# Performance work log

Measured on AMD Instinct MI355X. Metric: run time of the kernel, lower is better.

The kernel has to match this reference:

```python
import jax, jax.numpy as jnp
import numpy as np

G = 8   # channel groups
K = 4   # top-k per group


def setup_inputs() -> dict:
    key = jax.random.key(0)
    ks = jax.random.split(key, 6)
    B, C, H, W = 16, 256, 128, 128
    x = jax.random.normal(ks[0], (B, C, H, W), dtype=jnp.float32)
    # 1x1 conv weights (kernel dims squeezed):
    soft_w1 = jax.random.normal(ks[1], (G, C // G), dtype=jnp.float32) * 0.1  # grouped Conv2d(C, G, 1, groups=G)
    soft_w2 = jax.random.normal(ks[2], (C, G), dtype=jnp.float32) * 0.1       # Conv2d(G, C, 1)
    top_w1 = jax.random.normal(ks[3], (G, K), dtype=jnp.float32) * 0.1        # grouped Conv2d(G*K, G, 1, groups=G)
    top_w2 = jax.random.normal(ks[4], (C, G), dtype=jnp.float32) * 0.1        # Conv2d(G, C, 1)
    r = jax.random.normal(ks[5], (2,), dtype=jnp.float32)                     # branch mixing logits
    return {"x": x, "soft_w1": soft_w1, "soft_w2": soft_w2,
            "top_w1": top_w1, "top_w2": top_w2, "r": r}


def reference(x, soft_w1, soft_w2, top_w1, top_w2, r):
    B, C, H, W = x.shape
    Cg = C // G
    xg = x.reshape(B, G, Cg, H, W)

    # --- CGSoftmax branch: x + conv2(conv1(x * softmax_per_group(x))) ---
    att = jax.nn.softmax(xg, axis=2)          # softmax over within-group channels
    xs = xg * att                              # MulRes
    y = jnp.einsum('bgchw,gc->bghw', xs, soft_w1)     # grouped 1x1 conv C->G
    soft_out = x + jnp.einsum('bghw,og->bohw', y, soft_w2)  # 1x1 conv G->C, AddRes

    # --- CGTopK branch: x + conv2(conv1(topk_per_group(x))) ---
    tk = -jnp.sort(-xg, axis=2)[:, :, :K]      # top-K values, sorted descending: [B,G,K,H,W]
    yt = jnp.einsum('bgkhw,gk->bghw', tk, top_w1)     # grouped 1x1 conv G*K->G
    top_out = x + jnp.einsum('bghw,og->bohw', yt, top_w2)  # 1x1 conv G->C, AddRes

    # --- softmax-weighted branch combine ---
    w = jax.nn.softmax(r)
    rt, rs = w[0], w[1]
    return top_out * rt + soft_out * rs
```

## Files before the change

### kernel.cpp

```cpp
#include <hip/hip_runtime.h>
#include <math.h>


#define G_ 8
#define K_ 4
#define CG_ 32
#define C_ 256
#define HW_ (128 * 128)

typedef __attribute__((ext_vector_type(2))) float f32x2;

__launch_bounds__(512, 4)
__global__ void cgblock_kernel(const float* __restrict__ x,
                               const float* __restrict__ soft_w1,
                               const float* __restrict__ soft_w2,
                               const float* __restrict__ top_w1,
                               const float* __restrict__ top_w2,
                               const float* __restrict__ r,
                               float* __restrict__ out) {
    __shared__ f32x2 Ys[G_][64];
    __shared__ f32x2 Yt[G_][64];

    const int lane = threadIdx.x & 63;
    const int g = __builtin_amdgcn_readfirstlane(threadIdx.x >> 6);
    const int blk = blockIdx.x;
    const int b = blk >> 7;
    const int s = ((blk & 127) << 7) | (lane << 1);

    const long base = (long)(b * C_ + g * CG_) * HW_ + s;
    const f32x2* xp = (const f32x2*)(x + base);

    const float e0 = __expf(r[0]);
    const float e1 = __expf(r[1]);
    const float rt = e0 / (e0 + e1);
    const float rs = e1 / (e0 + e1);

    float va[CG_], vb[CG_];
#pragma unroll
    for (int c = 0; c < CG_; ++c) {
        const f32x2 L = __builtin_nontemporal_load(xp + c * (HW_ / 2));
        va[c] = L.x;
        vb[c] = L.y;
    }

    float ma = va[0], mb = vb[0];
#pragma unroll
    for (int c = 1; c < CG_; ++c) {
        ma = fmaxf(ma, va[c]);
        mb = fmaxf(mb, vb[c]);
    }
    float Za = 0.f, Zb = 0.f, aa = 0.f, ab = 0.f;
#pragma unroll
    for (int c = 0; c < CG_; ++c) {
        const float w1 = soft_w1[g * CG_ + c];
        const float ea = __expf(va[c] - ma);
        const float eb = __expf(vb[c] - mb);
        Za += ea;
        Zb += eb;
        aa = fmaf(va[c] * ea, w1, aa);
        ab = fmaf(vb[c] * eb, w1, ab);
    }
    const float ysa = aa / Za;
    const float ysb = ab / Zb;

    float a0 = -INFINITY, a1 = -INFINITY, a2 = -INFINITY, a3 = -INFINITY;
    float b0 = -INFINITY, b1 = -INFINITY, b2 = -INFINITY, b3 = -INFINITY;
#pragma unroll
    for (int c = 0; c < CG_; ++c) {
        float u = va[c];
        float d0 = fminf(a0, u); a0 = fmaxf(a0, u);
        float d1 = fminf(a1, d0); a1 = fmaxf(a1, d0);
        float d2 = fminf(a2, d1); a2 = fmaxf(a2, d1);
        a3 = fmaxf(a3, d2);
        u = vb[c];
        d0 = fminf(b0, u); b0 = fmaxf(b0, u);
        d1 = fminf(b1, d0); b1 = fmaxf(b1, d0);
        d2 = fminf(b2, d1); b2 = fmaxf(b2, d1);
        b3 = fmaxf(b3, d2);
    }
    const float tw0 = top_w1[g * K_ + 0], tw1 = top_w1[g * K_ + 1];
    const float tw2 = top_w1[g * K_ + 2], tw3 = top_w1[g * K_ + 3];
    const float yta = a0 * tw0 + a1 * tw1 + a2 * tw2 + a3 * tw3;
    const float ytb = b0 * tw0 + b1 * tw1 + b2 * tw2 + b3 * tw3;

    Ys[g][lane] = f32x2{ysa * rs, ysb * rs};
    Yt[g][lane] = f32x2{yta * rt, ytb * rt};
    __syncthreads();

    const float* w2s = soft_w2 + g * CG_ * G_;
    const float* w2t = top_w2 + g * CG_ * G_;
#pragma unroll
    for (int gg = 0; gg < G_; ++gg) {
        const f32x2 yf = Ys[gg][lane];
        const f32x2 tf = Yt[gg][lane];
#pragma unroll
        for (int c = 0; c < CG_; ++c) {
            const float cs = w2s[c * G_ + gg];
            const float ct = w2t[c * G_ + gg];
            va[c] = fmaf(cs, yf.x, va[c]);
            vb[c] = fmaf(cs, yf.y, vb[c]);
            va[c] = fmaf(ct, tf.x, va[c]);
            vb[c] = fmaf(ct, tf.y, vb[c]);
        }
    }

    f32x2* op = (f32x2*)(out + base);
#pragma unroll
    for (int c = 0; c < CG_; ++c) {
        __builtin_nontemporal_store(f32x2{va[c], vb[c]}, op + c * (HW_ / 2));
    }
}

extern "C" void kernel_launch(void* const* d_in, const int* in_sizes, int n_in,
                              void* d_out, int out_size, void* d_ws, size_t ws_size,
                              hipStream_t stream) {
    const float* x       = (const float*)d_in[0];
    const float* soft_w1 = (const float*)d_in[1];
    const float* soft_w2 = (const float*)d_in[2];
    const float* top_w1  = (const float*)d_in[3];
    const float* top_w2  = (const float*)d_in[4];
    const float* r       = (const float*)d_in[5];
    float* out = (float*)d_out;

    cgblock_kernel<<<dim3(2048), dim3(512), 0, stream>>>(
        x, soft_w1, soft_w2, top_w1, top_w2, r, out);
}
```

Measured before the change: 443.4 us.

## Vectorize compute with packed f32x2 math, med3 top-k, and interleaved store loop

Rewrites the per-pixel math on f32x2 vectors so the compiler can emit packed FMA/max instructions, replaces the min/max top-4 insertion network with fmed3-based updates, and turns the max reduction into a tree. The Ys/Yt shared arrays are merged into a single f32x4 array that is read once into registers. The output loop is reordered to finish and store each channel in turn, which frees registers earlier and overlaps stores with compute. The kernel is memory-bound, so the gain from reduced ALU work may be small; the extra yv registers could raise register pressure.

Result: no change. 435.9 us (-1.7%).

```diff
diff --git a/kernel.cpp b/kernel.cpp
--- a/kernel.cpp
+++ b/kernel.cpp
@@ -9,6 +9,22 @@
 #define HW_ (128 * 128)
 
 typedef __attribute__((ext_vector_type(2))) float f32x2;
+typedef __attribute__((ext_vector_type(4))) float f32x4;
+
+static __device__ __forceinline__ f32x2 pk2(float s) { return f32x2{s, s}; }
+
+static __device__ __forceinline__ f32x2 maxv(f32x2 a, f32x2 b) {
+    return __builtin_elementwise_max(a, b);
+}
+
+static __device__ __forceinline__ f32x2 fmav(f32x2 a, f32x2 b, f32x2 c) {
+    return __builtin_elementwise_fma(a, b, c);
+}
+
+static __device__ __forceinline__ f32x2 med3v(f32x2 u, f32x2 x, f32x2 y) {
+    return f32x2{__builtin_amdgcn_fmed3f(u.x, x.x, y.x),
+                 __builtin_amdgcn_fmed3f(u.y, x.y, y.y)};
+}
 
 __launch_bounds__(512, 4)
 __global__ void cgblock_kernel(const float* __restrict__ x,
@@ -18,8 +34,7 @@
                                const float* __restrict__ top_w2,
                                const float* __restrict__ r,
                                float* __restrict__ out) {
-    __shared__ f32x2 Ys[G_][64];
-    __shared__ f32x2 Yt[G_][64];
+    __shared__ f32x4 Y[G_][64];
 
     const int lane = threadIdx.x & 63;
     const int g = __builtin_amdgcn_readfirstlane(threadIdx.x >> 6);
@@ -35,79 +50,76 @@
     const float rt = e0 / (e0 + e1);
     const float rs = e1 / (e0 + e1);
 
-    float va[CG_], vb[CG_];
+    f32x2 v[CG_];
 #pragma unroll
     for (int c = 0; c < CG_; ++c) {
-        const f32x2 L = __builtin_nontemporal_load(xp + c * (HW_ / 2));
-        va[c] = L.x;
-        vb[c] = L.y;
+        v[c] = __builtin_nontemporal_load(xp + c * (HW_ / 2));
     }
 
-    float ma = va[0], mb = vb[0];
+    f32x2 mm[16];
 #pragma unroll
-    for (int c = 1; c < CG_; ++c) {
-        ma = fmaxf(ma, va[c]);
-        mb = fmaxf(mb, vb[c]);
+    for (int i = 0; i < 16; ++i) mm[i] = maxv(v[i], v[i + 16]);
+#pragma unroll
+    for (int st = 8; st >= 1; st >>= 1) {
+#pragma unroll
+        for (int i = 0; i < st; ++i) mm[i] = maxv(mm[i], mm[i + st]);
     }
-    float Za = 0.f, Zb = 0.f, aa = 0.f, ab = 0.f;
+    const f32x2 m = mm[0];
+
+    f32x2 Z = pk2(0.f), acc = pk2(0.f);
 #pragma unroll
     for (int c = 0; c < CG_; ++c) {
         const float w1 = soft_w1[g * CG_ + c];
-        const float ea = __expf(va[c] - ma);
-        const float eb = __expf(vb[c] - mb);
-        Za += ea;
-        Zb += eb;
-        aa = fmaf(va[c] * ea, w1, aa);
-        ab = fmaf(vb[c] * eb, w1, ab);
+        const f32x2 d = v[c] - m;
+        const f32x2 e = f32x2{__expf(d.x), __expf(d.y)};
+        Z += e;
+        acc = fmav(v[c] * e, pk2(w1), acc);
     }
-    const float ysa = aa / Za;
-    const float ysb = ab / Zb;
+    const f32x2 ys = f32x2{acc.x / Z.x, acc.y / Z.y};
 
-    float a0 = -INFINITY, a1 = -INFINITY, a2 = -INFINITY, a3 = -INFINITY;
-    float b0 = -INFINITY, b1 = -INFINITY, b2 = -INFINITY, b3 = -INFINITY;
+    f32x2 A0 = pk2(-INFINITY), A1 = pk2(-INFINITY);
+    f32x2 A2 = pk2(-INFINITY), A3 = pk2(-INFINITY);
 #pragma unroll
     for (int c = 0; c < CG_; ++c) {
-        float u = va[c];
-        float d0 = fminf(a0, u); a0 = fmaxf(a0, u);
-        float d1 = fminf(a1, d0); a1 = fmaxf(a1, d0);
-        float d2 = fminf(a2, d1); a2 = fmaxf(a2, d1);
-        a3 = fmaxf(a3, d2);
-        u = vb[c];
-        d0 = fminf(b0, u); b0 = fmaxf(b0, u);
-        d1 = fminf(b1, d0); b1 = fmaxf(b1, d0);
-        d2 = fminf(b2, d1); b2 = fmaxf(b2, d1);
-        b3 = fmaxf(b3, d2);
+        const f32x2 u = v[c];
+        const f32x2 n0 = maxv(A0, u);
+        const f32x2 n1 = med3v(u, A0, A1);
+        const f32x2 n2 = med3v(u, A1, A2);
+        const f32x2 n3 = med3v(u, A2, A3);
+        A0 = n0; A1 = n1; A2 = n2; A3 = n3;
     }
     const float tw0 = top_w1[g * K_ + 0], tw1 = top_w1[g * K_ + 1];
     const float tw2 = top_w1[g * K_ + 2], tw3 = top_w1[g * K_ + 3];
-    const float yta = a0 * tw0 + a1 * tw1 + a2 * tw2 + a3 * tw3;
-    const float ytb = b0 * tw0 + b1 * tw1 + b2 * tw2 + b3 * tw3;
+    f32x2 yt = A3 * pk2(tw3);
+    yt = fmav(A2, pk2(tw2), yt);
+    yt = fmav(A1, pk2(tw1), yt);
+    yt = fmav(A0, pk2(tw0), yt);
 
-    Ys[g][lane] = f32x2{ysa * rs, ysb * rs};
-    Yt[g][lane] = f32x2{yta * rt, ytb * rt};
+    const f32x2 yss = ys * pk2(rs);
+    const f32x2 ytt = yt * pk2(rt);
+    Y[g][lane] = f32x4{yss.x, yss.y, ytt.x, ytt.y};
     __syncthreads();
 
+    f32x4 yv[G_];
+#pragma unroll
+    for (int gg = 0; gg < G_; ++gg) yv[gg] = Y[gg][lane];
+
+    f32x2* op = (f32x2*)(out + base);
     const float* w2s = soft_w2 + g * CG_ * G_;
     const float* w2t = top_w2 + g * CG_ * G_;
 #pragma unroll
-    for (int gg = 0; gg < G_; ++gg) {
-        const f32x2 yf = Ys[gg][lane];
-        const f32x2 tf = Yt[gg][lane];
+    for (int c = 0; c < CG_; ++c) {
+        f32x2 o = v[c];
 #pragma unroll
-        for (int c = 0; c < CG_; ++c) {
+        for (int gg = 0; gg < G_; ++gg) {
             const float cs = w2s[c * G_ + gg];
             const float ct = w2t[c * G_ + gg];
-            va[c] = fmaf(cs, yf.x, va[c]);
-            vb[c] = fmaf(cs, yf.y, vb[c]);
-            va[c] = fmaf(ct, tf.x, va[c]);
-            vb[c] = fmaf(ct, tf.y, vb[c]);
+            const f32x2 yf = f32x2{yv[gg].x, yv[gg].y};
+            const f32x2 tf = f32x2{yv[gg].z, yv[gg].w};
+            o = fmav(pk2(cs), yf, o);
+            o = fmav(pk2(ct), tf, o);
         }
-    }
-
-    f32x2* op = (f32x2*)(out + base);
-#pragma unroll
-    for (int c = 0; c < CG_; ++c) {
-        __builtin_nontemporal_store(f32x2{va[c], vb[c]}, op + c * (HW_ / 2));
+        __builtin_nontemporal_store(o, op + c * (HW_ / 2));
     }
 }
 
```
